# Kernel tuning notes

Measured on AMD Instinct MI355X. Metric: run time of the kernel, lower is better.

## Reference

```python
import jax, jax.numpy as jnp
import numpy as np

D_MODEL = 1024
HEADS = 16
D_K = D_MODEL // HEADS
THETA = 10000.0
NEG = -1.0e9


def _rope(t, offset=0):
    # t: [B, H, S, D]; standard interleaved rotary embedding, base THETA
    S, D = t.shape[-2], t.shape[-1]
    half = D // 2
    inv_freq = 1.0 / (THETA ** (jnp.arange(half, dtype=jnp.float32) * 2.0 / D))
    pos = jnp.arange(offset, offset + S, dtype=jnp.float32)
    ang = pos[:, None] * inv_freq[None, :]          # [S, half]
    cos, sin = jnp.cos(ang), jnp.sin(ang)
    t1, t2 = t[..., ::2], t[..., 1::2]              # even / odd lanes
    o1 = t1 * cos - t2 * sin
    o2 = t1 * sin + t2 * cos
    return jnp.stack([o1, o2], axis=-1).reshape(t.shape)


def setup_inputs() -> dict:
    key = jax.random.key(0)
    k0, k1, k2, k3, k4 = jax.random.split(key, 5)
    B, S = 2, 2048
    x = jax.random.normal(k0, (B, S, D_MODEL), dtype=jnp.float32)
    att_mask = jnp.ones((B, S), dtype=jnp.int32)
    scale = 0.02
    wq = jax.random.normal(k1, (D_MODEL, D_MODEL), dtype=jnp.float32) * scale
    wk = jax.random.normal(k2, (D_MODEL, D_MODEL), dtype=jnp.float32) * scale
    wv = jax.random.normal(k3, (D_MODEL, D_MODEL), dtype=jnp.float32) * scale
    wo = jax.random.normal(k4, (D_MODEL, D_MODEL), dtype=jnp.float32) * scale
    return {"x": x, "att_mask": att_mask, "wq": wq, "wk": wk, "wv": wv, "wo": wo}


def reference(x, att_mask, wq, wk, wv, wo):
    B, S, _ = x.shape
    # nn.Linear(bias=False): y = x @ W^T ; then split heads -> [B, H, S, d_k]
    q = (x @ wq.T).reshape(B, S, HEADS, D_K).transpose(0, 2, 1, 3)
    k = (x @ wk.T).reshape(B, S, HEADS, D_K).transpose(0, 2, 1, 3)
    v = (x @ wv.T).reshape(B, S, HEADS, D_K).transpose(0, 2, 1, 3)
    # use_rope=True, start_pos=0, use_cache=False path
    q = _rope(q)
    k = _rope(k)
    scores = jnp.einsum("bhqd,bhkd->bhqk", q, k) / np.sqrt(D_K).astype(np.float32)
    pad = (att_mask == 0)[:, None, None, :]          # [B,1,1,S]
    scores = jnp.where(pad, NEG, scores)
    causal = jnp.tril(jnp.ones((S, S), dtype=bool))  # [S, S]
    scores = jnp.where(causal, scores, NEG)
    att = jax.nn.softmax(scores, axis=-1)
    ctx = jnp.einsum("bhqk,bhkd->bhqd", att, v)      # [B,H,S,d_k]
    final = ctx.transpose(0, 2, 1, 3).reshape(B, S, HEADS * D_K)
    return final @ wo.T
```

## Files before the change

kernel.cpp:

```cpp
#include <hip/hip_runtime.h>
#include <hip/hip_bf16.h>
#include <cstdint>

typedef unsigned short u16;
typedef __bf16 bf16x8 __attribute__((ext_vector_type(8)));
typedef float f32x4 __attribute__((ext_vector_type(4)));

#define S_LEN 2048
#define NH 16
#define DK 64
#define DM 1024

__device__ __forceinline__ u16 f2bf(float f) {
  union { float f; uint32_t u; } c; c.f = f;
  uint32_t u = c.u;
  u += 0x7fffu + ((u >> 16) & 1u);
  return (u16)(u >> 16);
}

__device__ __forceinline__ void gl_lds16(const void* gsrc, void* ldst) {
  __builtin_amdgcn_global_load_lds(
      (const __attribute__((address_space(1))) unsigned int*)gsrc,
      (__attribute__((address_space(3))) unsigned int*)ldst,
      16, 0, 0);
}

#define MFMA16(a, b, c) __builtin_amdgcn_mfma_f32_16x16x32_bf16((a), (b), (c), 0, 0, 0)
#define VMW(N) asm volatile("s_waitcnt vmcnt(" #N ")" ::: "memory")
#define BARM() asm volatile("s_barrier" ::: "memory")

__global__ __launch_bounds__(256) void prep_all(
    const float* x, const float* wq, const float* wk, const float* wv, const float* wo,
    const int* amask,
    u16* xb, u16* wqb, u16* wkb, u16* wvb, u16* wob, float2* tab, int* mflag)
{
  const int bid = blockIdx.x;
  if (bid < 2048) {
#pragma unroll
    for (int it = 0; it < 4; ++it) {
      size_t i = ((size_t)bid * 256 + threadIdx.x) * 4 + (size_t)it * 2097152u;
      const float* src; u16* dst; size_t off;
      if (i < 4194304u)      { src = x;  dst = xb;  off = i; }
      else if (i < 5242880u) { src = wq; dst = wqb; off = i - 4194304u; }
      else if (i < 6291456u) { src = wk; dst = wkb; off = i - 5242880u; }
      else if (i < 7340032u) { src = wv; dst = wvb; off = i - 6291456u; }
      else                   { src = wo; dst = wob; off = i - 7340032u; }
      float4 v = *(const float4*)(src + off);
      ushort4 o;
      o.x = f2bf(v.x); o.y = f2bf(v.y); o.z = f2bf(v.z); o.w = f2bf(v.w);
      *(ushort4*)(dst + off) = o;
    }
  } else if (bid < 2304) {
    int i = (bid - 2048) * 256 + threadIdx.x;
    int pos = i >> 5, f = i & 31;
    float inv = powf(10000.0f, -(float)f / 32.0f);
    float ang = (float)pos * inv;
    tab[i] = make_float2(cosf(ang), sinf(ang));
  } else {
    const int f = bid - 2304;
    if (threadIdx.x < 64) {
      const int b = f >> 5, t = f & 31;
      int v = amask[b * S_LEN + t * 64 + threadIdx.x];
      int all = (int)__all(v != 0);
      if (threadIdx.x == 0) mflag[f] = all;
    }
  }
}

__global__ __launch_bounds__(256, 4) void gemm_qkv32(
    const u16* xb, const u16* wqb, const u16* wkb, const u16* wvb,
    const float2* tab, u16* Qr, u16* Kr, u16* Vt)
{
  __shared__ __align__(16) u16 ldsA[2][128 * 32];
  __shared__ __align__(16) u16 ldsB[2][128 * 32];

  const int bid = blockIdx.x;
  const int xcd = bid & 7, v = bid >> 3;
  const int m0 = (xcd * 4 + (v & 3)) * 128;
  const int nc = v >> 2;
  const int z = nc >> 3;
  const int n0z = (nc & 7) * 128;
  const u16* Wz = (z == 0) ? wqb : ((z == 1) ? wkb : wvb);

  const int tid = threadIdx.x;
  const int w = tid >> 6, lane = tid & 63;
  const int l15 = lane & 15, g = lane >> 4;
  const int wm = (w >> 1) * 64, wn = (w & 1) * 64;
  const int lr4 = lane >> 2;
  const int scolb = ((lane & 3) * 16) ^ ((lr4 & 3) << 4);

  f32x4 acc[4][4] = {};

  auto stage = [&](int buf, int kt) {
#pragma unroll
    for (int c = 0; c < 2; ++c) {
      const int rb = c * 64 + w * 16;
      const int row = rb + lr4;
      gl_lds16((const char*)(xb + (size_t)(m0 + row) * DM + kt) + scolb,
               (char*)&ldsA[buf][0] + rb * 64);
      gl_lds16((const char*)(Wz + (size_t)(n0z + row) * DM + kt) + scolb,
               (char*)&ldsB[buf][0] + rb * 64);
    }
  };

  stage(0, 0);
  int cur = 0;
  for (int kt = 0; kt < DM; kt += 32) {
    if (kt + 32 < DM) { stage(cur ^ 1, kt + 32); VMW(4); } else { VMW(0); }
    BARM();
    bf16x8 af[4], bfr[4];
#pragma unroll
    for (int i = 0; i < 4; ++i) {
      const int ar = wm + i * 16 + l15;
      af[i] = *(const bf16x8*)((const char*)&ldsA[cur][0] + ar * 64 +
                               ((g * 16) ^ ((ar & 3) << 4)));
      const int br = wn + i * 16 + l15;
      bfr[i] = *(const bf16x8*)((const char*)&ldsB[cur][0] + br * 64 +
                                ((g * 16) ^ ((br & 3) << 4)));
    }
    __builtin_amdgcn_s_setprio(1);
#pragma unroll
    for (int i = 0; i < 4; ++i)
#pragma unroll
      for (int j = 0; j < 4; ++j)
        acc[i][j] = MFMA16(af[i], bfr[j], acc[i][j]);
    __builtin_amdgcn_s_setprio(0);
    BARM();
    cur ^= 1;
  }

  u16* dst = (z == 0) ? Qr : Kr;
#pragma unroll
  for (int i = 0; i < 4; ++i) {
#pragma unroll
    for (int j = 0; j < 4; ++j) {
      const int n = n0z + wn + j * 16 + l15;
      const int h = n >> 6, d = n & 63;
#pragma unroll
      for (int r = 0; r < 4; ++r) {
        const int m = m0 + wm + i * 16 + g * 4 + r;
        const int b = m >> 11, s = m & 2047;
        float vv = acc[i][j][r];
        if (z < 2) {
          float p = __shfl_xor(vv, 1);
          float2 cs = tab[s * 32 + (d >> 1)];
          float o = vv * cs.x + ((d & 1) ? p : -p) * cs.y;
          if (z == 0) o *= 0.18033688011f;
          dst[((size_t)(b * NH + h) * S_LEN + s) * DK + d] = f2bf(o);
        } else {
          Vt[((size_t)(b * NH + h) * DK + d) * S_LEN + s] = f2bf(vv);
        }
      }
    }
  }
}

__global__ __launch_bounds__(256, 4) void gemm_out64(const u16* ctx, const u16* wob, float* out) {
  __shared__ __align__(16) u16 ldsA[2][128 * 32];
  __shared__ __align__(16) u16 ldsB[2][64 * 32];

  const int bid = blockIdx.x;
  const int xcd = bid & 7, v = bid >> 3;
  const int m0 = (xcd * 4 + (v & 3)) * 128;
  const int n0 = (v >> 2) * 64;

  const int tid = threadIdx.x;
  const int w = tid >> 6, lane = tid & 63;
  const int l15 = lane & 15, g = lane >> 4;
  const int wm = (w >> 1) * 64, wn = (w & 1) * 32;
  const int lr4 = lane >> 2;
  const int scolb = ((lane & 3) * 16) ^ ((lr4 & 3) << 4);

  f32x4 acc[4][2] = {};

  auto stage = [&](int buf, int kt) {
#pragma unroll
    for (int c = 0; c < 2; ++c) {
      const int rb = c * 64 + w * 16;
      const int row = rb + lr4;
      gl_lds16((const char*)(ctx + (size_t)(m0 + row) * DM + kt) + scolb,
               (char*)&ldsA[buf][0] + rb * 64);
    }
    const int rb = w * 16;
    const int row = rb + lr4;
    gl_lds16((const char*)(wob + (size_t)(n0 + row) * DM + kt) + scolb,
             (char*)&ldsB[buf][0] + rb * 64);
  };

  stage(0, 0);
  int cur = 0;
  for (int kt = 0; kt < DM; kt += 32) {
    if (kt + 32 < DM) { stage(cur ^ 1, kt + 32); VMW(3); } else { VMW(0); }
    BARM();
    bf16x8 af[4], bfr[2];
#pragma unroll
    for (int i = 0; i < 4; ++i) {
      const int ar = wm + i * 16 + l15;
      af[i] = *(const bf16x8*)((const char*)&ldsA[cur][0] + ar * 64 +
                               ((g * 16) ^ ((ar & 3) << 4)));
    }
#pragma unroll
    for (int j = 0; j < 2; ++j) {
      const int br = wn + j * 16 + l15;
      bfr[j] = *(const bf16x8*)((const char*)&ldsB[cur][0] + br * 64 +
                                ((g * 16) ^ ((br & 3) << 4)));
    }
    __builtin_amdgcn_s_setprio(1);
#pragma unroll
    for (int i = 0; i < 4; ++i)
#pragma unroll
      for (int j = 0; j < 2; ++j)
        acc[i][j] = MFMA16(af[i], bfr[j], acc[i][j]);
    __builtin_amdgcn_s_setprio(0);
    BARM();
    cur ^= 1;
  }

#pragma unroll
  for (int i = 0; i < 4; ++i)
#pragma unroll
    for (int j = 0; j < 2; ++j)
#pragma unroll
      for (int r = 0; r < 4; ++r)
        out[(size_t)(m0 + wm + i * 16 + g * 4 + r) * DM + n0 + wn + j * 16 + l15] = acc[i][j][r];
}

__global__ __launch_bounds__(512, 4) void attn13(
    const u16* Qr, const u16* Kr, const u16* Vt, const int* amask, const int* mflag,
    u16* ctx)
{
  __shared__ __align__(16) u16 ldsK[2][64 * 64];
  __shared__ __align__(16) u16 ldsV[2][64 * 64];
  __shared__ __align__(16) __bf16 plds[8][16 * 72];

  const int bh = blockIdx.x;
  const int band = 15 - blockIdx.y;
  const int b = bh >> 4, h = bh & 15;
  const int tid = threadIdx.x, w8 = tid >> 6, lane = tid & 63;
  const int l15 = lane & 15, g = lane >> 4;
  const int r8 = lane >> 3;
  const int sw = ((lane & 7) * 16) ^ (r8 << 4);

  const int chunk = band * 4 + (w8 >> 1);
  const int q0 = chunk * 32 + (w8 & 1) * 16;
  const int myNt = (chunk >> 1) + 1;
  const int dTile = chunk >> 1;
  const int ntB = band * 2 + 2;

  const u16* Kb0 = Kr + (size_t)bh * S_LEN * DK;
  const u16* Vb0 = Vt + (size_t)bh * DK * S_LEN;
  const u16* Qb  = Qr + (size_t)bh * S_LEN * DK;

  bf16x8 qa0 = *(const bf16x8*)(Qb + (size_t)(q0 + l15) * DK + g * 8);
  bf16x8 qa1 = *(const bf16x8*)(Qb + (size_t)(q0 + l15) * DK + 32 + g * 8);

  union { u16 u[8]; bf16x8 v; } one_u;
#pragma unroll
  for (int i = 0; i < 8; ++i) one_u.u[i] = 0x3F80;
  const bf16x8 ones = one_u.v;

  float m[4];
  f32x4 lacc = {0.f, 0.f, 0.f, 0.f};
  f32x4 o[4];
#pragma unroll
  for (int r = 0; r < 4; ++r) m[r] = -3e38f;
#pragma unroll
  for (int dt = 0; dt < 4; ++dt) o[dt] = (f32x4){0.f, 0.f, 0.f, 0.f};

  auto stage = [&](int buf, int t) {
    const size_t kv0 = (size_t)t * 64;
    const int row = w8 * 8 + r8;
    gl_lds16((const char*)(Kb0 + (kv0 + row) * DK) + sw,
             (char*)&ldsK[buf][0] + (w8 * 8) * 128);
    gl_lds16((const char*)(Vb0 + (size_t)row * S_LEN + kv0) + sw,
             (char*)&ldsV[buf][0] + (w8 * 8) * 128);
  };

  stage(0, 0);
  int cur = 0;

  for (int t = 0; t < ntB; ++t) {
    if (t + 1 < ntB) { stage(cur ^ 1, t + 1); VMW(2); } else { VMW(0); }
    BARM();
    if (t < myNt) {
      const int kv0 = t * 64;
      const bool allok = mflag[(b << 5) + t] != 0;

      bf16x8 kb[4][2];
#pragma unroll
      for (int nt = 0; nt < 4; ++nt) {
        const int row = nt * 16 + l15;
#pragma unroll
        for (int ks = 0; ks < 2; ++ks)
          kb[nt][ks] = *(const bf16x8*)((const char*)&ldsK[cur][0] + row * 128 +
                                        ((ks * 64 + g * 16) ^ ((row & 7) << 4)));
      }
      f32x4 s[4];
#pragma unroll
      for (int nt = 0; nt < 4; ++nt) s[nt] = (f32x4){0.f, 0.f, 0.f, 0.f};
      __builtin_amdgcn_s_setprio(1);
#pragma unroll
      for (int nt = 0; nt < 4; ++nt) {
        s[nt] = MFMA16(qa0, kb[nt][0], s[nt]);
        s[nt] = MFMA16(qa1, kb[nt][1], s[nt]);
      }
      __builtin_amdgcn_s_setprio(0);

      if (!allok) {
#pragma unroll
        for (int nt = 0; nt < 4; ++nt) {
          const int pmv = amask[b * S_LEN + kv0 + nt * 16 + l15];
#pragma unroll
          for (int r = 0; r < 4; ++r)
            if (!pmv) s[nt][r] = -1e9f;
        }
      }
      if (t == dTile) {
#pragma unroll
        for (int nt = 0; nt < 4; ++nt) {
          const int kvc = kv0 + nt * 16 + l15;
#pragma unroll
          for (int r = 0; r < 4; ++r)
            s[nt][r] = (kvc <= q0 + g * 4 + r) ? s[nt][r] : -1e9f;
        }
      }

      float tmax[4];
      bool need = false;
#pragma unroll
      for (int r = 0; r < 4; ++r) {
        float t0 = fmaxf(fmaxf(s[0][r], s[1][r]), fmaxf(s[2][r], s[3][r]));
        t0 = fmaxf(t0, __shfl_xor(t0, 1));
        t0 = fmaxf(t0, __shfl_xor(t0, 2));
        t0 = fmaxf(t0, __shfl_xor(t0, 4));
        t0 = fmaxf(t0, __shfl_xor(t0, 8));
        tmax[r] = t0;
        need = need || (t0 > m[r] + 11.5415603f);
      }
      if (__any((int)need)) {
#pragma unroll
        for (int r = 0; r < 4; ++r) {
          const float mnew = fmaxf(m[r], tmax[r]);
          const float alpha = exp2f(m[r] - mnew);
          m[r] = mnew;
          lacc[r] *= alpha;
#pragma unroll
          for (int dt = 0; dt < 4; ++dt) o[dt][r] *= alpha;
        }
      }
      __bf16* pw = &plds[w8][0];
#pragma unroll
      for (int r = 0; r < 4; ++r) {
#pragma unroll
        for (int nt = 0; nt < 4; ++nt)
          pw[(g * 4 + r) * 72 + nt * 16 + l15] = (__bf16)exp2f(s[nt][r] - m[r]);
      }
      bf16x8 pa0 = *(const bf16x8*)(pw + l15 * 72 + g * 8);
      bf16x8 pa1 = *(const bf16x8*)(pw + l15 * 72 + 32 + g * 8);
      bf16x8 vb[4][2];
#pragma unroll
      for (int dt = 0; dt < 4; ++dt) {
        const int row = dt * 16 + l15;
#pragma unroll
        for (int ks = 0; ks < 2; ++ks)
          vb[dt][ks] = *(const bf16x8*)((const char*)&ldsV[cur][0] + row * 128 +
                                        ((ks * 64 + g * 16) ^ ((row & 7) << 4)));
      }
      __builtin_amdgcn_s_setprio(1);
      lacc = MFMA16(pa0, ones, lacc);
      lacc = MFMA16(pa1, ones, lacc);
#pragma unroll
      for (int dt = 0; dt < 4; ++dt) {
        o[dt] = MFMA16(pa0, vb[dt][0], o[dt]);
        o[dt] = MFMA16(pa1, vb[dt][1], o[dt]);
      }
      __builtin_amdgcn_s_setprio(0);
    }
    BARM();
    cur ^= 1;
  }

#pragma unroll
  for (int dt = 0; dt < 4; ++dt)
#pragma unroll
    for (int r = 0; r < 4; ++r) {
      const int q = q0 + g * 4 + r;
      ctx[((size_t)(b * S_LEN + q)) * DM + h * DK + dt * 16 + l15] =
          f2bf(o[dt][r] / lacc[r]);
    }
}

extern "C" void kernel_launch(void* const* d_in, const int* in_sizes, int n_in,
                              void* d_out, int out_size, void* d_ws, size_t ws_size,
                              hipStream_t stream) {
  const float* x   = (const float*)d_in[0];
  const int* amask = (const int*)d_in[1];
  const float* wq  = (const float*)d_in[2];
  const float* wk  = (const float*)d_in[3];
  const float* wv  = (const float*)d_in[4];
  const float* wo  = (const float*)d_in[5];
  float* out = (float*)d_out;

  char* ws = (char*)d_ws;
  u16* xb    = (u16*)(ws);
  u16* wqb   = (u16*)(ws + ( 8u << 20));
  u16* wkb   = (u16*)(ws + (10u << 20));
  u16* wvb   = (u16*)(ws + (12u << 20));
  u16* wob   = (u16*)(ws + (14u << 20));
  float2* tab = (float2*)(ws + (16u << 20));
  int* mflag = (int*)(ws + (16u << 20) + (768u << 10));
  u16* Qr    = (u16*)(ws + (17u << 20));
  u16* Kr    = (u16*)(ws + (25u << 20));
  u16* Vt    = (u16*)(ws + (33u << 20));
  u16* ctx   = (u16*)(ws + (41u << 20));

  hipLaunchKernelGGL(prep_all, dim3(2368), dim3(256), 0, stream,
                     x, wq, wk, wv, wo, amask, xb, wqb, wkb, wvb, wob, tab, mflag);
  hipLaunchKernelGGL(gemm_qkv32, dim3(768), dim3(256), 0, stream,
                     xb, wqb, wkb, wvb, tab, Qr, Kr, Vt);
  hipLaunchKernelGGL(attn13, dim3(32, 16), dim3(512), 0, stream,
                     Qr, Kr, Vt, amask, mflag, ctx);
  hipLaunchKernelGGL(gemm_out64, dim3(512), dim3(256), 0, stream, ctx, wob, out);
}
```

Measured before the change: 144.6 us.

## Shrink attention blocks to 4 waves over 64-query bands with swizzled P buffer

```diff
diff --git a/kernel.cpp b/kernel.cpp
--- a/kernel.cpp
+++ b/kernel.cpp
@@ -225,27 +225,25 @@
         out[(size_t)(m0 + wm + i * 16 + g * 4 + r) * DM + n0 + wn + j * 16 + l15] = acc[i][j][r];
 }
 
-__global__ __launch_bounds__(512, 4) void attn13(
+__global__ __launch_bounds__(256, 4) void attn14(
     const u16* Qr, const u16* Kr, const u16* Vt, const int* amask, const int* mflag,
     u16* ctx)
 {
   __shared__ __align__(16) u16 ldsK[2][64 * 64];
   __shared__ __align__(16) u16 ldsV[2][64 * 64];
-  __shared__ __align__(16) __bf16 plds[8][16 * 72];
+  __shared__ __align__(16) __bf16 plds[4][16 * 64];
 
   const int bh = blockIdx.x;
-  const int band = 15 - blockIdx.y;
+  const int band = 31 - blockIdx.y;
   const int b = bh >> 4, h = bh & 15;
-  const int tid = threadIdx.x, w8 = tid >> 6, lane = tid & 63;
+  const int tid = threadIdx.x, w = tid >> 6, lane = tid & 63;
   const int l15 = lane & 15, g = lane >> 4;
   const int r8 = lane >> 3;
   const int sw = ((lane & 7) * 16) ^ (r8 << 4);
 
-  const int chunk = band * 4 + (w8 >> 1);
-  const int q0 = chunk * 32 + (w8 & 1) * 16;
-  const int myNt = (chunk >> 1) + 1;
-  const int dTile = chunk >> 1;
-  const int ntB = band * 2 + 2;
+  const int q0 = band * 64 + w * 16;
+  const int dTile = band;
+  const int ntB = band + 1;
 
   const u16* Kb0 = Kr + (size_t)bh * S_LEN * DK;
   const u16* Vb0 = Vt + (size_t)bh * DK * S_LEN;
@@ -269,20 +267,24 @@
 
   auto stage = [&](int buf, int t) {
     const size_t kv0 = (size_t)t * 64;
-    const int row = w8 * 8 + r8;
-    gl_lds16((const char*)(Kb0 + (kv0 + row) * DK) + sw,
-             (char*)&ldsK[buf][0] + (w8 * 8) * 128);
-    gl_lds16((const char*)(Vb0 + (size_t)row * S_LEN + kv0) + sw,
-             (char*)&ldsV[buf][0] + (w8 * 8) * 128);
+#pragma unroll
+    for (int c = 0; c < 2; ++c) {
+      const int rb = w * 16 + c * 8;
+      const int row = rb + r8;
+      gl_lds16((const char*)(Kb0 + (kv0 + row) * DK) + sw,
+               (char*)&ldsK[buf][0] + rb * 128);
+      gl_lds16((const char*)(Vb0 + (size_t)row * S_LEN + kv0) + sw,
+               (char*)&ldsV[buf][0] + rb * 128);
+    }
   };
 
   stage(0, 0);
   int cur = 0;
 
   for (int t = 0; t < ntB; ++t) {
-    if (t + 1 < ntB) { stage(cur ^ 1, t + 1); VMW(2); } else { VMW(0); }
-    BARM();
-    if (t < myNt) {
+    if (t + 1 < ntB) { stage(cur ^ 1, t + 1); VMW(4); } else { VMW(0); }
+    BARM();
+    {
       const int kv0 = t * 64;
       const bool allok = mflag[(b << 5) + t] != 0;
 
@@ -348,15 +350,17 @@
           for (int dt = 0; dt < 4; ++dt) o[dt][r] *= alpha;
         }
       }
-      __bf16* pw = &plds[w8][0];
+      __bf16* pw = &plds[w][0];
 #pragma unroll
       for (int r = 0; r < 4; ++r) {
+        const int row = g * 4 + r;
 #pragma unroll
         for (int nt = 0; nt < 4; ++nt)
-          pw[(g * 4 + r) * 72 + nt * 16 + l15] = (__bf16)exp2f(s[nt][r] - m[r]);
-      }
-      bf16x8 pa0 = *(const bf16x8*)(pw + l15 * 72 + g * 8);
-      bf16x8 pa1 = *(const bf16x8*)(pw + l15 * 72 + 32 + g * 8);
+          pw[row * 64 + ((nt * 16 + l15) ^ ((row & 7) << 3))] =
+              (__bf16)exp2f(s[nt][r] - m[r]);
+      }
+      bf16x8 pa0 = *(const bf16x8*)(pw + l15 * 64 + ((g * 8) ^ ((l15 & 7) << 3)));
+      bf16x8 pa1 = *(const bf16x8*)(pw + l15 * 64 + ((32 + g * 8) ^ ((l15 & 7) << 3)));
       bf16x8 vb[4][2];
 #pragma unroll
       for (int dt = 0; dt < 4; ++dt) {
@@ -418,7 +422,7 @@
                      x, wq, wk, wv, wo, amask, xb, wqb, wkb, wvb, wob, tab, mflag);
   hipLaunchKernelGGL(gemm_qkv32, dim3(768), dim3(256), 0, stream,
                      xb, wqb, wkb, wvb, tab, Qr, Kr, Vt);
-  hipLaunchKernelGGL(attn13, dim3(32, 16), dim3(512), 0, stream,
+  hipLaunchKernelGGL(attn14, dim3(32, 32), dim3(256), 0, stream,
                      Qr, Kr, Vt, amask, mflag, ctx);
   hipLaunchKernelGGL(gemm_out64, dim3(512), dim3(256), 0, stream, ctx, wob, out);
 }
```

New measurement: 137.8 us. -4.8%, faster.
